# Optimization experiments

Measured on AMD Instinct MI355X. Metric: run time of the kernel, lower is better.

Reference implementation:

```python
import jax, jax.numpy as jnp
import numpy as np

B, H, S, D = 2, 16, 2048, 64

def setup_inputs() -> dict:
    key = jax.random.key(0)
    kq, kk, kv = jax.random.split(key, 3)
    q = jax.random.normal(kq, (B, H, S, D), dtype=jnp.float32)
    k = jax.random.normal(kk, (B, H, S, D), dtype=jnp.float32)
    v = jax.random.normal(kv, (B, H, S, D), dtype=jnp.float32)
    mask = jnp.tril(jnp.ones((S, S), dtype=bool))  # causal, broadcast over B,H
    return {"q": q, "k": k, "v": v, "mask": mask}

def reference(q, k, v, mask):
    d_k = q.shape[-1]
    # [..., num_q, num_kv]
    qk = jnp.einsum('bhqd,bhkd->bhqk', q, k) / jnp.sqrt(jnp.asarray(d_k, q.dtype))
    qk = jnp.where(mask, qk, -jnp.inf)
    attn = jax.nn.softmax(qk, axis=-1)
    return jnp.einsum('bhqk,bhkd->bhqd', attn, v)
```

## Files before the change

### kernel.cpp

```cpp
#include <hip/hip_runtime.h>

#define SS 2048
#define DD 64
#define BH 32
#define M_SUB 16.0f
#define QSCALE 0.1803368801f
#define NCHUNK 40
#define NSLOT (BH * NCHUNK)

typedef __attribute__((ext_vector_type(8))) short short8;
typedef __attribute__((ext_vector_type(4))) float floatx4;

__device__ __forceinline__ short f2bf(float x) {
  union { float f; unsigned u; } un; un.f = x;
  unsigned r = (un.u + 0x7FFFu + ((un.u >> 16) & 1u)) >> 16;
  return (short)r;
}
__device__ __forceinline__ short f2bf_fast(float x) {
  union { float f; unsigned u; } un; un.f = x;
  return (short)((un.u + 0x8000u) >> 16);
}
__device__ __forceinline__ float fexp2(float x) {
  return __builtin_amdgcn_exp2f(x);
}
__device__ __forceinline__ void gload16(const short* g, short* l) {
  __builtin_amdgcn_global_load_lds(
      (const __attribute__((address_space(1))) void*)g,
      (__attribute__((address_space(3))) void*)l, 16, 0, 0);
}
#define MFMA __builtin_amdgcn_mfma_f32_16x16x32_bf16

__global__ __launch_bounds__(256) void prep_k(const float* __restrict__ K,
                                              short* __restrict__ Kbf) {
  const size_t i = ((size_t)blockIdx.x * 256 + threadIdx.x) * 8;
  floatx4 a = *(const floatx4*)(K + i);
  floatx4 b = *(const floatx4*)(K + i + 4);
  short8 s;
  s[0]=f2bf(a[0]); s[1]=f2bf(a[1]); s[2]=f2bf(a[2]); s[3]=f2bf(a[3]);
  s[4]=f2bf(b[0]); s[5]=f2bf(b[1]); s[6]=f2bf(b[2]); s[7]=f2bf(b[3]);
  *(short8*)(Kbf + i) = s;
}

__device__ __forceinline__ int kperm(int c) {
  return (((c >> 2) & 1) << 4) + ((c >> 3) << 2) + (c & 3);
}

__global__ __launch_bounds__(256) void prep_vtp(const float* __restrict__ V,
                                                short* __restrict__ Vtp) {
  __shared__ short Ts[64][72];
  const int bh = blockIdx.y;
  const int s0 = blockIdx.x * 64;
  const int t = threadIdx.x;
  {
    const int r = t >> 2, c = (t & 3) * 16;
    const float* g = V + ((size_t)bh * SS + s0 + r) * DD + c;
    floatx4 a = *(const floatx4*)g;
    floatx4 b = *(const floatx4*)(g + 4);
    floatx4 cc = *(const floatx4*)(g + 8);
    floatx4 d = *(const floatx4*)(g + 12);
    short8 x0, x1;
    x0[0]=f2bf(a[0]); x0[1]=f2bf(a[1]); x0[2]=f2bf(a[2]); x0[3]=f2bf(a[3]);
    x0[4]=f2bf(b[0]); x0[5]=f2bf(b[1]); x0[6]=f2bf(b[2]); x0[7]=f2bf(b[3]);
    x1[0]=f2bf(cc[0]);x1[1]=f2bf(cc[1]);x1[2]=f2bf(cc[2]);x1[3]=f2bf(cc[3]);
    x1[4]=f2bf(d[0]); x1[5]=f2bf(d[1]); x1[6]=f2bf(d[2]); x1[7]=f2bf(d[3]);
    *(short8*)&Ts[r][c] = x0;
    *(short8*)&Ts[r][c + 8] = x1;
  }
  __syncthreads();
  {
    const int d = t >> 2, cblk = (t & 3) * 16;
    short8 y0, y1;
    #pragma unroll
    for (int j = 0; j < 8; ++j) {
      const int c0 = cblk + j, c1 = cblk + 8 + j;
      y0[j] = Ts[(c0 & 32) + kperm(c0 & 31)][d];
      y1[j] = Ts[(c1 & 32) + kperm(c1 & 31)][d];
    }
    const int kt  = (s0 + cblk) >> 5;
    const int kin = cblk & 31;
    short* o = Vtp + (((size_t)bh * 64 + kt) * 64 + d) * 32 + kin;
    *(short8*)o = y0;
    *(short8*)(o + 8) = y1;
  }
}

__device__ __forceinline__ void y2qc(int y, int& qt, int& c) {
  if (y < 4)       { qt = y;                            c = 0; }
  else if (y < 12) { int i = y - 4;  qt = 4 + (i >> 1); c = i & 1; }
  else if (y < 24) { int i = y - 12; qt = 8 + i / 3;    c = i - (qt - 8) * 3; }
  else             { int i = y - 24; qt = 12 + (i >> 2); c = i & 3; }
}

__global__ __launch_bounds__(256, 4) void sdpa_part(
    const float* __restrict__ Q, const short* __restrict__ Kbf,
    const short* __restrict__ Vtp, float* __restrict__ PO,
    float* __restrict__ PRS) {
  __shared__ __align__(16) short Sh[2][4224];

  const int tid  = threadIdx.x;
  const int w    = tid >> 6;
  const int lane = tid & 63;
  const int quad = lane >> 4;
  const int l16  = lane & 15;

  const int bh = blockIdx.x;
  const int y  = 39 - (int)blockIdx.y;
  int qt, c; y2qc(y, qt, c);
  const int kt0 = c * 16;
  const int kt1 = min(kt0 + 16, 4 * qt + 4);
  const int ktd = 4 * qt + w;
  const int qA  = qt * 128 + w * 32;
  const int qB  = qA + 16;

  const size_t base = (size_t)bh * SS * DD;
  const short* kbase = Kbf + base;
  const short* vtb   = Vtp + (size_t)bh * 64 * 2048;

  {
    const short* gk = kbase + (size_t)kt0 * 2048 + w * 512 + lane * 8;
    gload16(gk, &Sh[0][w * 544]);
    const short* gv = vtb + (size_t)kt0 * 2048 + w * 512 + lane * 8;
    gload16(gv, &Sh[0][2176 + w * 512]);
  }

  short8 qaA0, qaA1, qaB0, qaB1;
  {
    const float* ga = Q + base + (size_t)(qA + l16) * DD + quad * 8;
    const float* gb = Q + base + (size_t)(qB + l16) * DD + quad * 8;
    floatx4 a0 = *(const floatx4*)ga,        a1 = *(const floatx4*)(ga + 4);
    floatx4 a2 = *(const floatx4*)(ga + 32), a3 = *(const floatx4*)(ga + 36);
    floatx4 b0 = *(const floatx4*)gb,        b1 = *(const floatx4*)(gb + 4);
    floatx4 b2 = *(const floatx4*)(gb + 32), b3 = *(const floatx4*)(gb + 36);
    #pragma unroll
    for (int j = 0; j < 4; ++j) {
      qaA0[j] = f2bf(a0[j] * QSCALE); qaA0[4 + j] = f2bf(a1[j] * QSCALE);
      qaA1[j] = f2bf(a2[j] * QSCALE); qaA1[4 + j] = f2bf(a3[j] * QSCALE);
      qaB0[j] = f2bf(b0[j] * QSCALE); qaB0[4 + j] = f2bf(b1[j] * QSCALE);
      qaB1[j] = f2bf(b2[j] * QSCALE); qaB1[4 + j] = f2bf(b3[j] * QSCALE);
    }
  }

  floatx4 z = {0.f, 0.f, 0.f, 0.f};
  floatx4 oA0 = z, oA1 = z, oA2 = z, oA3 = z;
  floatx4 oB0 = z, oB1 = z, oB2 = z, oB3 = z;
  float rsA = 0.f, rsB = 0.f;

  __asm__ volatile("s_waitcnt vmcnt(0)" ::: "memory");
  __syncthreads();

  int nb = 0;
  for (int kt = kt0; kt < kt1; ++kt) {
    if (kt + 1 < kt1) {
      const short* gk = kbase + (size_t)(kt + 1) * 2048 + w * 512 + lane * 8;
      gload16(gk, &Sh[nb ^ 1][w * 544]);
      const short* gv = vtb + (size_t)(kt + 1) * 2048 + w * 512 + lane * 8;
      gload16(gv, &Sh[nb ^ 1][2176 + w * 512]);
    }

    if (kt <= ktd) {
      const short* lb = Sh[nb];
      const int kro = (l16 & 7) * 64 + quad * 8;
      const int kc  = (l16 >> 3) * 544;
      short8 kb00 = *(const short8*)(lb + kc + kro);
      short8 kb01 = *(const short8*)(lb + kc + kro + 32);
      short8 kb10 = *(const short8*)(lb + kc + 1088 + kro);
      short8 kb11 = *(const short8*)(lb + kc + 1088 + kro + 32);
      const int vro = 2176 + l16 * 32 + quad * 8;
      short8 vt0 = *(const short8*)(lb + vro);
      short8 vt1 = *(const short8*)(lb + vro + 512);
      short8 vt2 = *(const short8*)(lb + vro + 1024);
      short8 vt3 = *(const short8*)(lb + vro + 1536);

      floatx4 tA0 = z, tA1 = z, tB0 = z, tB1 = z;
      tA0 = MFMA(kb00, qaA0, tA0, 0, 0, 0); tA0 = MFMA(kb01, qaA1, tA0, 0, 0, 0);
      tA1 = MFMA(kb10, qaA0, tA1, 0, 0, 0); tA1 = MFMA(kb11, qaA1, tA1, 0, 0, 0);
      tB0 = MFMA(kb00, qaB0, tB0, 0, 0, 0); tB0 = MFMA(kb01, qaB1, tB0, 0, 0, 0);
      tB1 = MFMA(kb10, qaB0, tB1, 0, 0, 0); tB1 = MFMA(kb11, qaB1, tB1, 0, 0, 0);

      if (kt == ktd) {
        const int kq = quad * 4;
        #pragma unroll
        for (int r = 0; r < 4; ++r) {
          tA0[r] = (kq + r      <= l16)      ? tA0[r] : -1e30f;
          tA1[r] = (kq + r + 16 <= l16)      ? tA1[r] : -1e30f;
          tB0[r] = (kq + r      <= l16 + 16) ? tB0[r] : -1e30f;
          tB1[r] = (kq + r      <= l16)      ? tB1[r] : -1e30f;
        }
      }

      short8 paA, paB;
      #pragma unroll
      for (int r = 0; r < 4; ++r) {
        const float pA0 = fexp2(tA0[r] - M_SUB), pA1 = fexp2(tA1[r] - M_SUB);
        const float pB0 = fexp2(tB0[r] - M_SUB), pB1 = fexp2(tB1[r] - M_SUB);
        rsA += pA0 + pA1;
        rsB += pB0 + pB1;
        paA[r] = f2bf_fast(pA0); paA[4 + r] = f2bf_fast(pA1);
        paB[r] = f2bf_fast(pB0); paB[4 + r] = f2bf_fast(pB1);
      }

      oA0 = MFMA(vt0, paA, oA0, 0, 0, 0); oA1 = MFMA(vt1, paA, oA1, 0, 0, 0);
      oA2 = MFMA(vt2, paA, oA2, 0, 0, 0); oA3 = MFMA(vt3, paA, oA3, 0, 0, 0);
      oB0 = MFMA(vt0, paB, oB0, 0, 0, 0); oB1 = MFMA(vt1, paB, oB1, 0, 0, 0);
      oB2 = MFMA(vt2, paB, oB2, 0, 0, 0); oB3 = MFMA(vt3, paB, oB3, 0, 0, 0);
    }

    __asm__ volatile("s_waitcnt vmcnt(0)" ::: "memory");
    __syncthreads();
    nb ^= 1;
  }

  rsA += __shfl_xor(rsA, 16, 64); rsA += __shfl_xor(rsA, 32, 64);
  rsB += __shfl_xor(rsB, 16, 64); rsB += __shfl_xor(rsB, 32, 64);

  const int slot = bh * NCHUNK + y;
  float* po = PO + (size_t)slot * (128 * 64);
  float* ra = po + (w * 32 + l16) * 64 + quad * 4;
  float* rb = po + (w * 32 + 16 + l16) * 64 + quad * 4;
  *(floatx4*)(ra)      = oA0;
  *(floatx4*)(ra + 16) = oA1;
  *(floatx4*)(ra + 32) = oA2;
  *(floatx4*)(ra + 48) = oA3;
  *(floatx4*)(rb)      = oB0;
  *(floatx4*)(rb + 16) = oB1;
  *(floatx4*)(rb + 32) = oB2;
  *(floatx4*)(rb + 48) = oB3;
  if (quad == 0) {
    PRS[slot * 128 + w * 32 + l16]      = rsA;
    PRS[slot * 128 + w * 32 + 16 + l16] = rsB;
  }
}

__global__ __launch_bounds__(256) void sdpa_combine(
    const float* __restrict__ PO, const float* __restrict__ PRS,
    float* __restrict__ O) {
  const int bh  = blockIdx.x;
  const int g32 = blockIdx.y;
  const int qt  = g32 >> 2;
  const int t   = threadIdx.x;
  const int row  = t >> 3;
  const int col  = (t & 7) * 8;
  const int rloc = (g32 & 3) * 32 + row;

  const int g  = qt >> 2;
  const int cn = g + 1;
  int ybase;
  if      (g == 0) ybase = qt;
  else if (g == 1) ybase = 4 + 2 * (qt - 4);
  else if (g == 2) ybase = 12 + 3 * (qt - 8);
  else             ybase = 24 + 4 * (qt - 12);

  floatx4 accL = {0.f,0.f,0.f,0.f}, accH = accL;
  float den = 0.f;
  for (int c = 0; c < cn; ++c) {
    const int slot = bh * NCHUNK + ybase + c;
    const float* po = PO + (size_t)slot * (128 * 64) + rloc * 64 + col;
    floatx4 a = *(const floatx4*)po;
    floatx4 b = *(const floatx4*)(po + 4);
    accL += a; accH += b;
    den += PRS[slot * 128 + rloc];
  }
  const float inv = 1.0f / den;
  accL *= inv; accH *= inv;
  float* out = O + ((size_t)bh * SS + qt * 128 + rloc) * DD + col;
  *(floatx4*)out = accL;
  *(floatx4*)(out + 4) = accH;
}

extern "C" void kernel_launch(void* const* d_in, const int* in_sizes, int n_in,
                              void* d_out, int out_size, void* d_ws, size_t ws_size,
                              hipStream_t stream) {
  (void)in_sizes; (void)n_in; (void)out_size; (void)ws_size;
  const float* q = (const float*)d_in[0];
  const float* k = (const float*)d_in[1];
  const float* v = (const float*)d_in[2];
  float* o = (float*)d_out;

  short* Kbf = (short*)d_ws;
  short* Vtp = Kbf + (size_t)BH * SS * DD;
  float* PO  = (float*)(Vtp + (size_t)BH * SS * DD);
  float* PRS = PO + (size_t)NSLOT * 128 * 64;

  prep_k<<<dim3(BH * SS * DD / 8 / 256), 256, 0, stream>>>(k, Kbf);
  prep_vtp<<<dim3(SS / 64, BH), 256, 0, stream>>>(v, Vtp);
  sdpa_part<<<dim3(BH, NCHUNK), 256, 0, stream>>>(q, Kbf, Vtp, PO, PRS);
  sdpa_combine<<<dim3(BH, SS / 32), 256, 0, stream>>>(PO, PRS, o);
}
```

Baseline: 143.5 us.

## Halve waves per block, give each wave 64 query rows, triple-buffer K/V

The attention partial kernel now runs 2 waves per block instead of 4, and each wave handles four 16-row query sub-tiles (64 rows). Each K/V tile read from LDS is therefore reused across more queries. The shared-memory ring grows from two to three buffers, and the barrier moves to the top of the loop. Wave 0 loads K while wave 1 loads V. The aim is less LDS read traffic and fewer barriers per unit of work, at the cost of more registers per wave (four sets of accumulators), fewer waves to hide latency, and a larger LDS footprint.

```diff
diff --git a/kernel.cpp b/kernel.cpp
--- a/kernel.cpp
+++ b/kernel.cpp
@@ -7,6 +7,7 @@
 #define QSCALE 0.1803368801f
 #define NCHUNK 40
 #define NSLOT (BH * NCHUNK)
+#define BUFS 4224
 
 typedef __attribute__((ext_vector_type(8))) short short8;
 typedef __attribute__((ext_vector_type(4))) float floatx4;
@@ -91,11 +92,11 @@
   else             { int i = y - 24; qt = 12 + (i >> 2); c = i & 3; }
 }
 
-__global__ __launch_bounds__(256, 4) void sdpa_part(
+__global__ __launch_bounds__(128, 3) void sdpa_part(
     const float* __restrict__ Q, const short* __restrict__ Kbf,
     const short* __restrict__ Vtp, float* __restrict__ PO,
     float* __restrict__ PRS) {
-  __shared__ __align__(16) short Sh[2][4224];
+  __shared__ __align__(16) short Sh[3 * BUFS];
 
   const int tid  = threadIdx.x;
   const int w    = tid >> 6;
@@ -108,126 +109,132 @@
   int qt, c; y2qc(y, qt, c);
   const int kt0 = c * 16;
   const int kt1 = min(kt0 + 16, 4 * qt + 4);
-  const int ktd = 4 * qt + w;
-  const int qA  = qt * 128 + w * 32;
-  const int qB  = qA + 16;
+  const int qt4w = qt * 4 + w * 2;
+  const int ktdw = qt4w + 1;
 
   const size_t base = (size_t)bh * SS * DD;
   const short* kbase = Kbf + base;
   const short* vtb   = Vtp + (size_t)bh * 64 * 2048;
 
-  {
-    const short* gk = kbase + (size_t)kt0 * 2048 + w * 512 + lane * 8;
-    gload16(gk, &Sh[0][w * 544]);
-    const short* gv = vtb + (size_t)kt0 * 2048 + w * 512 + lane * 8;
-    gload16(gv, &Sh[0][2176 + w * 512]);
-  }
-
-  short8 qaA0, qaA1, qaB0, qaB1;
-  {
-    const float* ga = Q + base + (size_t)(qA + l16) * DD + quad * 8;
-    const float* gb = Q + base + (size_t)(qB + l16) * DD + quad * 8;
-    floatx4 a0 = *(const floatx4*)ga,        a1 = *(const floatx4*)(ga + 4);
-    floatx4 a2 = *(const floatx4*)(ga + 32), a3 = *(const floatx4*)(ga + 36);
-    floatx4 b0 = *(const floatx4*)gb,        b1 = *(const floatx4*)(gb + 4);
-    floatx4 b2 = *(const floatx4*)(gb + 32), b3 = *(const floatx4*)(gb + 36);
+  short8 qa0[4], qa1[4];
+  #pragma unroll
+  for (int s = 0; s < 4; ++s) {
+    const float* g = Q + base + (size_t)(qt * 128 + w * 64 + s * 16 + l16) * DD + quad * 8;
+    floatx4 x0 = *(const floatx4*)g,        x1 = *(const floatx4*)(g + 4);
+    floatx4 x2 = *(const floatx4*)(g + 32), x3 = *(const floatx4*)(g + 36);
     #pragma unroll
     for (int j = 0; j < 4; ++j) {
-      qaA0[j] = f2bf(a0[j] * QSCALE); qaA0[4 + j] = f2bf(a1[j] * QSCALE);
-      qaA1[j] = f2bf(a2[j] * QSCALE); qaA1[4 + j] = f2bf(a3[j] * QSCALE);
-      qaB0[j] = f2bf(b0[j] * QSCALE); qaB0[4 + j] = f2bf(b1[j] * QSCALE);
-      qaB1[j] = f2bf(b2[j] * QSCALE); qaB1[4 + j] = f2bf(b3[j] * QSCALE);
+      qa0[s][j] = f2bf(x0[j] * QSCALE); qa0[s][4 + j] = f2bf(x1[j] * QSCALE);
+      qa1[s][j] = f2bf(x2[j] * QSCALE); qa1[s][4 + j] = f2bf(x3[j] * QSCALE);
+    }
+  }
+
+  {
+    if (w == 0) {
+      const short* gk = kbase + (size_t)kt0 * 2048 + lane * 8;
+      #pragma unroll
+      for (int i = 0; i < 4; ++i) gload16(gk + i * 512, &Sh[i * 544]);
+    } else {
+      const short* gv = vtb + (size_t)kt0 * 2048 + lane * 8;
+      #pragma unroll
+      for (int i = 0; i < 4; ++i) gload16(gv + i * 512, &Sh[2176 + i * 512]);
     }
   }
 
   floatx4 z = {0.f, 0.f, 0.f, 0.f};
-  floatx4 oA0 = z, oA1 = z, oA2 = z, oA3 = z;
-  floatx4 oB0 = z, oB1 = z, oB2 = z, oB3 = z;
-  float rsA = 0.f, rsB = 0.f;
-
-  __asm__ volatile("s_waitcnt vmcnt(0)" ::: "memory");
-  __syncthreads();
-
-  int nb = 0;
+  floatx4 o0[4] = {z,z,z,z}, o1[4] = {z,z,z,z}, o2[4] = {z,z,z,z}, o3[4] = {z,z,z,z};
+  float rs[4] = {0.f, 0.f, 0.f, 0.f};
+
+  int cb = 0;
   for (int kt = kt0; kt < kt1; ++kt) {
+    __asm__ volatile("s_waitcnt vmcnt(0)" ::: "memory");
+    __syncthreads();
+
     if (kt + 1 < kt1) {
-      const short* gk = kbase + (size_t)(kt + 1) * 2048 + w * 512 + lane * 8;
-      gload16(gk, &Sh[nb ^ 1][w * 544]);
-      const short* gv = vtb + (size_t)(kt + 1) * 2048 + w * 512 + lane * 8;
-      gload16(gv, &Sh[nb ^ 1][2176 + w * 512]);
-    }
-
-    if (kt <= ktd) {
-      const short* lb = Sh[nb];
-      const int kro = (l16 & 7) * 64 + quad * 8;
-      const int kc  = (l16 >> 3) * 544;
-      short8 kb00 = *(const short8*)(lb + kc + kro);
-      short8 kb01 = *(const short8*)(lb + kc + kro + 32);
-      short8 kb10 = *(const short8*)(lb + kc + 1088 + kro);
-      short8 kb11 = *(const short8*)(lb + kc + 1088 + kro + 32);
+      const int nb = (cb == 2) ? 0 : cb + 1;
+      if (w == 0) {
+        const short* gk = kbase + (size_t)(kt + 1) * 2048 + lane * 8;
+        #pragma unroll
+        for (int i = 0; i < 4; ++i) gload16(gk + i * 512, &Sh[nb * BUFS + i * 544]);
+      } else {
+        const short* gv = vtb + (size_t)(kt + 1) * 2048 + lane * 8;
+        #pragma unroll
+        for (int i = 0; i < 4; ++i) gload16(gv + i * 512, &Sh[nb * BUFS + 2176 + i * 512]);
+      }
+    }
+
+    if (kt <= ktdw) {
+      const short* lb = &Sh[cb * BUFS];
+      const int c0 = (l16 >> 3) * 544 + (l16 & 7) * 64 + quad * 8;
+      short8 kb00 = *(const short8*)(lb + c0);
+      short8 kb01 = *(const short8*)(lb + c0 + 32);
+      short8 kb10 = *(const short8*)(lb + c0 + 1088);
+      short8 kb11 = *(const short8*)(lb + c0 + 1088 + 32);
       const int vro = 2176 + l16 * 32 + quad * 8;
       short8 vt0 = *(const short8*)(lb + vro);
       short8 vt1 = *(const short8*)(lb + vro + 512);
       short8 vt2 = *(const short8*)(lb + vro + 1024);
       short8 vt3 = *(const short8*)(lb + vro + 1536);
 
-      floatx4 tA0 = z, tA1 = z, tB0 = z, tB1 = z;
-      tA0 = MFMA(kb00, qaA0, tA0, 0, 0, 0); tA0 = MFMA(kb01, qaA1, tA0, 0, 0, 0);
-      tA1 = MFMA(kb10, qaA0, tA1, 0, 0, 0); tA1 = MFMA(kb11, qaA1, tA1, 0, 0, 0);
-      tB0 = MFMA(kb00, qaB0, tB0, 0, 0, 0); tB0 = MFMA(kb01, qaB1, tB0, 0, 0, 0);
-      tB1 = MFMA(kb10, qaB0, tB1, 0, 0, 0); tB1 = MFMA(kb11, qaB1, tB1, 0, 0, 0);
-
-      if (kt == ktd) {
-        const int kq = quad * 4;
-        #pragma unroll
-        for (int r = 0; r < 4; ++r) {
-          tA0[r] = (kq + r      <= l16)      ? tA0[r] : -1e30f;
-          tA1[r] = (kq + r + 16 <= l16)      ? tA1[r] : -1e30f;
-          tB0[r] = (kq + r      <= l16 + 16) ? tB0[r] : -1e30f;
-          tB1[r] = (kq + r      <= l16)      ? tB1[r] : -1e30f;
+      #pragma unroll
+      for (int s = 0; s < 4; ++s) {
+        const int diag = qt4w + (s >> 1);
+        if (kt <= diag) {
+          floatx4 t0 = z, t1 = z;
+          t0 = MFMA(kb00, qa0[s], t0, 0, 0, 0); t0 = MFMA(kb01, qa1[s], t0, 0, 0, 0);
+          t1 = MFMA(kb10, qa0[s], t1, 0, 0, 0); t1 = MFMA(kb11, qa1[s], t1, 0, 0, 0);
+          if (kt == diag) {
+            const int kq = quad * 4;
+            if ((s & 1) == 0) {
+              #pragma unroll
+              for (int r = 0; r < 4; ++r) {
+                t0[r] = (kq + r <= l16) ? t0[r] : -1e30f;
+                t1[r] = -1e30f;
+              }
+            } else {
+              #pragma unroll
+              for (int r = 0; r < 4; ++r)
+                t1[r] = (kq + r <= l16) ? t1[r] : -1e30f;
+            }
+          }
+          short8 pa;
+          #pragma unroll
+          for (int r = 0; r < 4; ++r) {
+            const float p0 = fexp2(t0[r] - M_SUB);
+            const float p1 = fexp2(t1[r] - M_SUB);
+            rs[s] += p0 + p1;
+            pa[r] = f2bf_fast(p0); pa[4 + r] = f2bf_fast(p1);
+          }
+          o0[s] = MFMA(vt0, pa, o0[s], 0, 0, 0);
+          o1[s] = MFMA(vt1, pa, o1[s], 0, 0, 0);
+          o2[s] = MFMA(vt2, pa, o2[s], 0, 0, 0);
+          o3[s] = MFMA(vt3, pa, o3[s], 0, 0, 0);
         }
       }
-
-      short8 paA, paB;
-      #pragma unroll
-      for (int r = 0; r < 4; ++r) {
-        const float pA0 = fexp2(tA0[r] - M_SUB), pA1 = fexp2(tA1[r] - M_SUB);
-        const float pB0 = fexp2(tB0[r] - M_SUB), pB1 = fexp2(tB1[r] - M_SUB);
-        rsA += pA0 + pA1;
-        rsB += pB0 + pB1;
-        paA[r] = f2bf_fast(pA0); paA[4 + r] = f2bf_fast(pA1);
-        paB[r] = f2bf_fast(pB0); paB[4 + r] = f2bf_fast(pB1);
-      }
-
-      oA0 = MFMA(vt0, paA, oA0, 0, 0, 0); oA1 = MFMA(vt1, paA, oA1, 0, 0, 0);
-      oA2 = MFMA(vt2, paA, oA2, 0, 0, 0); oA3 = MFMA(vt3, paA, oA3, 0, 0, 0);
-      oB0 = MFMA(vt0, paB, oB0, 0, 0, 0); oB1 = MFMA(vt1, paB, oB1, 0, 0, 0);
-      oB2 = MFMA(vt2, paB, oB2, 0, 0, 0); oB3 = MFMA(vt3, paB, oB3, 0, 0, 0);
-    }
-
-    __asm__ volatile("s_waitcnt vmcnt(0)" ::: "memory");
-    __syncthreads();
-    nb ^= 1;
-  }
-
-  rsA += __shfl_xor(rsA, 16, 64); rsA += __shfl_xor(rsA, 32, 64);
-  rsB += __shfl_xor(rsB, 16, 64); rsB += __shfl_xor(rsB, 32, 64);
+    }
+    cb = (cb == 2) ? 0 : cb + 1;
+  }
+
+  #pragma unroll
+  for (int s = 0; s < 4; ++s) {
+    rs[s] += __shfl_xor(rs[s], 16, 64);
+    rs[s] += __shfl_xor(rs[s], 32, 64);
+  }
 
   const int slot = bh * NCHUNK + y;
   float* po = PO + (size_t)slot * (128 * 64);
-  float* ra = po + (w * 32 + l16) * 64 + quad * 4;
-  float* rb = po + (w * 32 + 16 + l16) * 64 + quad * 4;
-  *(floatx4*)(ra)      = oA0;
-  *(floatx4*)(ra + 16) = oA1;
-  *(floatx4*)(ra + 32) = oA2;
-  *(floatx4*)(ra + 48) = oA3;
-  *(floatx4*)(rb)      = oB0;
-  *(floatx4*)(rb + 16) = oB1;
-  *(floatx4*)(rb + 32) = oB2;
-  *(floatx4*)(rb + 48) = oB3;
+  #pragma unroll
+  for (int s = 0; s < 4; ++s) {
+    float* ra = po + (w * 64 + s * 16 + l16) * 64 + quad * 4;
+    *(floatx4*)(ra)      = o0[s];
+    *(floatx4*)(ra + 16) = o1[s];
+    *(floatx4*)(ra + 32) = o2[s];
+    *(floatx4*)(ra + 48) = o3[s];
+  }
   if (quad == 0) {
-    PRS[slot * 128 + w * 32 + l16]      = rsA;
-    PRS[slot * 128 + w * 32 + 16 + l16] = rsB;
+    #pragma unroll
+    for (int s = 0; s < 4; ++s)
+      PRS[slot * 128 + w * 64 + s * 16 + l16] = rs[s];
   }
 }
 
@@ -283,6 +290,6 @@
 
   prep_k<<<dim3(BH * SS * DD / 8 / 256), 256, 0, stream>>>(k, Kbf);
   prep_vtp<<<dim3(SS / 64, BH), 256, 0, stream>>>(v, Vtp);
-  sdpa_part<<<dim3(BH, NCHUNK), 256, 0, stream>>>(q, Kbf, Vtp, PO, PRS);
+  sdpa_part<<<dim3(BH, NCHUNK), 128, 0, stream>>>(q, Kbf, Vtp, PO, PRS);
   sdpa_combine<<<dim3(BH, SS / 32), 256, 0, stream>>>(PO, PRS, o);
 }
```

After: 149.4 us. 1.04x slower.

## Process two KV tiles per barrier and compute row sums via MFMA

Applied to the files above, without the earlier changes.

The KV loop now stages two key/value tiles per double-buffer slot, which halves the number of waitcnt/barrier pairs per block at the cost of doubling LDS use per block. Row sums of the probabilities are now accumulated with an MFMA against a ones vector, replacing the scalar adds and the cross-lane shuffles. The constant max-subtraction (M_SUB) is dropped, so exponents are taken of raw scaled scores. This risks fp32/bf16 overflow if scores grow large, and the larger LDS footprint may limit occupancy under the 4-blocks launch bound. The row sums are now built from bf16-rounded probabilities, which changes precision slightly.

```diff
diff --git a/kernel.cpp b/kernel.cpp
--- a/kernel.cpp
+++ b/kernel.cpp
@@ -3,10 +3,10 @@
 #define SS 2048
 #define DD 64
 #define BH 32
-#define M_SUB 16.0f
 #define QSCALE 0.1803368801f
 #define NCHUNK 40
 #define NSLOT (BH * NCHUNK)
+#define BUFS 8448
 
 typedef __attribute__((ext_vector_type(8))) short short8;
 typedef __attribute__((ext_vector_type(4))) float floatx4;
@@ -95,7 +95,7 @@
     const float* __restrict__ Q, const short* __restrict__ Kbf,
     const short* __restrict__ Vtp, float* __restrict__ PO,
     float* __restrict__ PRS) {
-  __shared__ __align__(16) short Sh[2][4224];
+  __shared__ __align__(16) short Sh[2][BUFS];
 
   const int tid  = threadIdx.x;
   const int w    = tid >> 6;
@@ -118,9 +118,11 @@
 
   {
     const short* gk = kbase + (size_t)kt0 * 2048 + w * 512 + lane * 8;
-    gload16(gk, &Sh[0][w * 544]);
+    gload16(gk,        &Sh[0][w * 544]);
+    gload16(gk + 2048, &Sh[0][2176 + w * 544]);
     const short* gv = vtb + (size_t)kt0 * 2048 + w * 512 + lane * 8;
-    gload16(gv, &Sh[0][2176 + w * 512]);
+    gload16(gv,        &Sh[0][4352 + w * 512]);
+    gload16(gv + 2048, &Sh[0][6400 + w * 512]);
   }
 
   short8 qaA0, qaA1, qaB0, qaB1;
@@ -140,78 +142,83 @@
     }
   }
 
+  short8 ones;
+  #pragma unroll
+  for (int j = 0; j < 8; ++j) ones[j] = (short)0x3F80;
+
   floatx4 z = {0.f, 0.f, 0.f, 0.f};
   floatx4 oA0 = z, oA1 = z, oA2 = z, oA3 = z;
   floatx4 oB0 = z, oB1 = z, oB2 = z, oB3 = z;
-  float rsA = 0.f, rsB = 0.f;
-
-  __asm__ volatile("s_waitcnt vmcnt(0)" ::: "memory");
-  __syncthreads();
+  floatx4 sA = z, sB = z;
 
   int nb = 0;
-  for (int kt = kt0; kt < kt1; ++kt) {
-    if (kt + 1 < kt1) {
-      const short* gk = kbase + (size_t)(kt + 1) * 2048 + w * 512 + lane * 8;
-      gload16(gk, &Sh[nb ^ 1][w * 544]);
-      const short* gv = vtb + (size_t)(kt + 1) * 2048 + w * 512 + lane * 8;
-      gload16(gv, &Sh[nb ^ 1][2176 + w * 512]);
-    }
-
-    if (kt <= ktd) {
-      const short* lb = Sh[nb];
-      const int kro = (l16 & 7) * 64 + quad * 8;
-      const int kc  = (l16 >> 3) * 544;
-      short8 kb00 = *(const short8*)(lb + kc + kro);
-      short8 kb01 = *(const short8*)(lb + kc + kro + 32);
-      short8 kb10 = *(const short8*)(lb + kc + 1088 + kro);
-      short8 kb11 = *(const short8*)(lb + kc + 1088 + kro + 32);
-      const int vro = 2176 + l16 * 32 + quad * 8;
-      short8 vt0 = *(const short8*)(lb + vro);
-      short8 vt1 = *(const short8*)(lb + vro + 512);
-      short8 vt2 = *(const short8*)(lb + vro + 1024);
-      short8 vt3 = *(const short8*)(lb + vro + 1536);
-
-      floatx4 tA0 = z, tA1 = z, tB0 = z, tB1 = z;
-      tA0 = MFMA(kb00, qaA0, tA0, 0, 0, 0); tA0 = MFMA(kb01, qaA1, tA0, 0, 0, 0);
-      tA1 = MFMA(kb10, qaA0, tA1, 0, 0, 0); tA1 = MFMA(kb11, qaA1, tA1, 0, 0, 0);
-      tB0 = MFMA(kb00, qaB0, tB0, 0, 0, 0); tB0 = MFMA(kb01, qaB1, tB0, 0, 0, 0);
-      tB1 = MFMA(kb10, qaB0, tB1, 0, 0, 0); tB1 = MFMA(kb11, qaB1, tB1, 0, 0, 0);
-
-      if (kt == ktd) {
-        const int kq = quad * 4;
+  for (int ktp = kt0; ktp < kt1; ktp += 2) {
+    __asm__ volatile("s_waitcnt vmcnt(0)" ::: "memory");
+    __syncthreads();
+
+    if (ktp + 2 < kt1) {
+      const short* gk = kbase + (size_t)(ktp + 2) * 2048 + w * 512 + lane * 8;
+      gload16(gk,        &Sh[nb ^ 1][w * 544]);
+      gload16(gk + 2048, &Sh[nb ^ 1][2176 + w * 544]);
+      const short* gv = vtb + (size_t)(ktp + 2) * 2048 + w * 512 + lane * 8;
+      gload16(gv,        &Sh[nb ^ 1][4352 + w * 512]);
+      gload16(gv + 2048, &Sh[nb ^ 1][6400 + w * 512]);
+    }
+
+    #pragma unroll
+    for (int j = 0; j < 2; ++j) {
+      const int kt = ktp + j;
+      if (kt <= ktd) {
+        const short* lb = &Sh[nb][j * 2176];
+        const short* vb = &Sh[nb][4352 + j * 2048];
+        const int kro = (l16 >> 3) * 544 + (l16 & 7) * 64 + quad * 8;
+        short8 kb00 = *(const short8*)(lb + kro);
+        short8 kb01 = *(const short8*)(lb + kro + 32);
+        short8 kb10 = *(const short8*)(lb + kro + 1088);
+        short8 kb11 = *(const short8*)(lb + kro + 1120);
+        const int vro = l16 * 32 + quad * 8;
+        short8 vt0 = *(const short8*)(vb + vro);
+        short8 vt1 = *(const short8*)(vb + vro + 512);
+        short8 vt2 = *(const short8*)(vb + vro + 1024);
+        short8 vt3 = *(const short8*)(vb + vro + 1536);
+
+        floatx4 tA0 = z, tA1 = z, tB0 = z, tB1 = z;
+        tA0 = MFMA(kb00, qaA0, tA0, 0, 0, 0); tA0 = MFMA(kb01, qaA1, tA0, 0, 0, 0);
+        tA1 = MFMA(kb10, qaA0, tA1, 0, 0, 0); tA1 = MFMA(kb11, qaA1, tA1, 0, 0, 0);
+        tB0 = MFMA(kb00, qaB0, tB0, 0, 0, 0); tB0 = MFMA(kb01, qaB1, tB0, 0, 0, 0);
+        tB1 = MFMA(kb10, qaB0, tB1, 0, 0, 0); tB1 = MFMA(kb11, qaB1, tB1, 0, 0, 0);
+
+        if (kt == ktd) {
+          const int kq = quad * 4;
+          #pragma unroll
+          for (int r = 0; r < 4; ++r) {
+            tA0[r] = (kq + r      <= l16)      ? tA0[r] : -1e30f;
+            tA1[r] = (kq + r + 16 <= l16)      ? tA1[r] : -1e30f;
+            tB0[r] = (kq + r      <= l16 + 16) ? tB0[r] : -1e30f;
+            tB1[r] = (kq + r      <= l16)      ? tB1[r] : -1e30f;
+          }
+        }
+
+        short8 paA, paB;
         #pragma unroll
         for (int r = 0; r < 4; ++r) {
-          tA0[r] = (kq + r      <= l16)      ? tA0[r] : -1e30f;
-          tA1[r] = (kq + r + 16 <= l16)      ? tA1[r] : -1e30f;
-          tB0[r] = (kq + r      <= l16 + 16) ? tB0[r] : -1e30f;
-          tB1[r] = (kq + r      <= l16)      ? tB1[r] : -1e30f;
+          paA[r]     = f2bf_fast(fexp2(tA0[r]));
+          paA[4 + r] = f2bf_fast(fexp2(tA1[r]));
+          paB[r]     = f2bf_fast(fexp2(tB0[r]));
+          paB[4 + r] = f2bf_fast(fexp2(tB1[r]));
         }
+
+        sA = MFMA(ones, paA, sA, 0, 0, 0);
+        sB = MFMA(ones, paB, sB, 0, 0, 0);
+
+        oA0 = MFMA(vt0, paA, oA0, 0, 0, 0); oA1 = MFMA(vt1, paA, oA1, 0, 0, 0);
+        oA2 = MFMA(vt2, paA, oA2, 0, 0, 0); oA3 = MFMA(vt3, paA, oA3, 0, 0, 0);
+        oB0 = MFMA(vt0, paB, oB0, 0, 0, 0); oB1 = MFMA(vt1, paB, oB1, 0, 0, 0);
+        oB2 = MFMA(vt2, paB, oB2, 0, 0, 0); oB3 = MFMA(vt3, paB, oB3, 0, 0, 0);
       }
-
-      short8 paA, paB;
-      #pragma unroll
-      for (int r = 0; r < 4; ++r) {
-        const float pA0 = fexp2(tA0[r] - M_SUB), pA1 = fexp2(tA1[r] - M_SUB);
-        const float pB0 = fexp2(tB0[r] - M_SUB), pB1 = fexp2(tB1[r] - M_SUB);
-        rsA += pA0 + pA1;
-        rsB += pB0 + pB1;
-        paA[r] = f2bf_fast(pA0); paA[4 + r] = f2bf_fast(pA1);
-        paB[r] = f2bf_fast(pB0); paB[4 + r] = f2bf_fast(pB1);
-      }
-
-      oA0 = MFMA(vt0, paA, oA0, 0, 0, 0); oA1 = MFMA(vt1, paA, oA1, 0, 0, 0);
-      oA2 = MFMA(vt2, paA, oA2, 0, 0, 0); oA3 = MFMA(vt3, paA, oA3, 0, 0, 0);
-      oB0 = MFMA(vt0, paB, oB0, 0, 0, 0); oB1 = MFMA(vt1, paB, oB1, 0, 0, 0);
-      oB2 = MFMA(vt2, paB, oB2, 0, 0, 0); oB3 = MFMA(vt3, paB, oB3, 0, 0, 0);
-    }
-
-    __asm__ volatile("s_waitcnt vmcnt(0)" ::: "memory");
-    __syncthreads();
+    }
     nb ^= 1;
   }
-
-  rsA += __shfl_xor(rsA, 16, 64); rsA += __shfl_xor(rsA, 32, 64);
-  rsB += __shfl_xor(rsB, 16, 64); rsB += __shfl_xor(rsB, 32, 64);
 
   const int slot = bh * NCHUNK + y;
   float* po = PO + (size_t)slot * (128 * 64);
@@ -226,8 +233,8 @@
   *(floatx4*)(rb + 32) = oB2;
   *(floatx4*)(rb + 48) = oB3;
   if (quad == 0) {
-    PRS[slot * 128 + w * 32 + l16]      = rsA;
-    PRS[slot * 128 + w * 32 + 16 + l16] = rsB;
+    PRS[slot * 128 + w * 32 + l16]      = sA[0];
+    PRS[slot * 128 + w * 32 + 16 + l16] = sB[0];
   }
 }
 
```

After: 137.7 us. 1.04x faster.
